# Performance work log

Hardware: AMD Instinct MI355X
Metric: run time of the kernel (lower is better)

The kernel has to match this reference:

```python
import jax, jax.numpy as jnp
import numpy as np

B, T, C, H = 2, 2048, 1024, 16
D = C // H  # head dim = 64


def setup_inputs() -> dict:
    key = jax.random.key(0)
    ks = jax.random.split(key, 9)
    s = 1.0 / np.sqrt(C)
    x = jax.random.normal(ks[0], (B, T, C), dtype=jnp.float32)
    # causal lower-triangular mask, broadcast over heads: [B, 1, T, T]
    attn_mask = jnp.broadcast_to(jnp.tril(jnp.ones((T, T), dtype=jnp.int32)), (B, 1, T, T))
    Wq = jax.random.normal(ks[1], (C, C), dtype=jnp.float32) * s
    Wk = jax.random.normal(ks[2], (C, C), dtype=jnp.float32) * s
    Wv = jax.random.normal(ks[3], (C, C), dtype=jnp.float32) * s
    Wo = jax.random.normal(ks[4], (C, C), dtype=jnp.float32) * s
    bq = jax.random.normal(ks[5], (C,), dtype=jnp.float32) * s
    bk = jax.random.normal(ks[6], (C,), dtype=jnp.float32) * s
    bv = jax.random.normal(ks[7], (C,), dtype=jnp.float32) * s
    bo = jax.random.normal(ks[8], (C,), dtype=jnp.float32) * s
    return {"x": x, "attn_mask": attn_mask, "Wq": Wq, "bq": bq, "Wk": Wk, "bk": bk,
            "Wv": Wv, "bv": bv, "Wo": Wo, "bo": bo}


def reference(x, attn_mask, Wq, bq, Wk, bk, Wv, bv, Wo, bo):
    # Q/K/V projections: nn.Linear applies x @ W^T + b
    def split_heads(t):  # [B,T,C] -> [B,H,T,D]
        return t.reshape(B, T, H, D).transpose(0, 2, 1, 3)

    q = split_heads(x @ Wq.T + bq)
    k = split_heads(x @ Wk.T + bk)
    v = split_heads(x @ Wv.T + bv)

    scale = 1.0 / np.sqrt(D)
    att = jnp.einsum('bhqd,bhkd->bhqk', q, k) * scale  # [B,H,T,T]
    att = jnp.where(attn_mask[:, :, :T, :T] == 0, -jnp.inf, att)
    att = jax.nn.softmax(att, axis=-1)
    # dropout p=0.0 -> identity
    y = jnp.einsum('bhqk,bhkd->bhqd', att, v)  # [B,H,T,D]
    y = y.transpose(0, 2, 1, 3).reshape(B, T, C)
    return y @ Wo.T + bo
```

## Files before the change

### kernel.cpp

```cpp
#include <hip/hip_runtime.h>
#include <hip/hip_bf16.h>

#define B_ 2
#define T_ 2048
#define C_ 1024
#define H_ 16
#define D_ 64
#define BT_ (B_ * T_)
#define S3_ 3072

typedef __bf16 bf16x8 __attribute__((ext_vector_type(8)));
typedef short short8v __attribute__((ext_vector_type(8)));
typedef short s16x4 __attribute__((ext_vector_type(4)));
typedef float f32x4 __attribute__((ext_vector_type(4)));

__device__ inline bf16x8 ld_frag_bf(const short* p) {
    short8v s = *(const short8v*)p;
    return __builtin_bit_cast(bf16x8, s);
}
__device__ inline short f2bf(float f) {
    union { float f; unsigned u; } x;
    x.f = f;
    unsigned r = x.u + 0x7fff + ((x.u >> 16) & 1);
    return (short)(r >> 16);
}
__device__ inline void st_out(short* p, float v) { *p = f2bf(v); }
__device__ inline void st_out(float* p, float v) { *p = v; }

__device__ inline void async16(const void* g, void* l) {
    __builtin_amdgcn_global_load_lds(
        (const __attribute__((address_space(1))) unsigned*)g,
        (__attribute__((address_space(3))) unsigned*)l, 16, 0, 0);
}

__global__ __launch_bounds__(256) void conv_inputs(
    const float* __restrict__ x,
    const float* __restrict__ Wq, const float* __restrict__ Wk,
    const float* __restrict__ Wv, const float* __restrict__ Wo,
    short* __restrict__ xb, short* __restrict__ Wqkvb, short* __restrict__ Wob)
{
    size_t e = ((size_t)blockIdx.x * 256 + threadIdx.x) * 8;
    int r = (int)(e >> 20);
    size_t off = e & ((1u << 20) - 1);
    const float* src; short* dst;
    if (r < 4)      { src = x + e;  dst = xb + e; }
    else if (r < 7) { src = (r == 4 ? Wq : r == 5 ? Wk : Wv) + off;
                      dst = Wqkvb + ((size_t)(r - 4) << 20) + off; }
    else            { src = Wo + off; dst = Wob + off; }
    f32x4 a = *(const f32x4*)src;
    f32x4 b = *(const f32x4*)(src + 4);
    short8v s;
#pragma unroll
    for (int i = 0; i < 4; ++i) { s[i] = f2bf(a[i]); s[i + 4] = f2bf(b[i]); }
    *(short8v*)dst = s;
}

__global__ __launch_bounds__(256) void gemm_qkv(
    const short* __restrict__ A,
    const short* __restrict__ Wb,
    const float* __restrict__ b0, const float* __restrict__ b1,
    const float* __restrict__ b2,
    short* __restrict__ Out, short* __restrict__ VQ)
{
    constexpr int K = 1024;
    __shared__ __align__(16) short Bs[128 * 64];
    __shared__ __align__(16) short As[128 * 64];

    const int tid = threadIdx.x;
    const int w = tid >> 6, l = tid & 63;
    const int c = l & 15, qd = l >> 4;
    const int m0 = blockIdx.y * 128, n0 = blockIdx.x * 128;
    const int wm = w >> 1, wn = w & 1;
    const int srcC = (l & 7) ^ (l >> 3);

    f32x4 acc[4][4] = {};

    for (int k0 = 0; k0 < K; k0 += 64) {
#pragma unroll
        for (int p = 0; p < 4; ++p) {
            int row = (w * 4 + p) * 8 + (l >> 3);
            async16(Wb + (size_t)(n0 + row) * K + k0 + srcC * 8,
                    Bs + (w * 4 + p) * 512 + l * 8);
            async16(A + (size_t)(m0 + row) * K + k0 + srcC * 8,
                    As + (w * 4 + p) * 512 + l * 8);
        }
        __syncthreads();

#pragma unroll
        for (int h = 0; h < 2; ++h) {
            const int slot = ((h * 4 + qd) ^ (c & 7)) * 8;
            bf16x8 af[4], bfr[4];
#pragma unroll
            for (int i = 0; i < 4; ++i) {
                af[i]  = ld_frag_bf(As + (wm * 64 + i * 16 + c) * 64 + slot);
                bfr[i] = ld_frag_bf(Bs + (wn * 64 + i * 16 + c) * 64 + slot);
            }
#pragma unroll
            for (int i = 0; i < 4; ++i)
#pragma unroll
                for (int j = 0; j < 4; ++j)
                    acc[i][j] = __builtin_amdgcn_mfma_f32_16x16x32_bf16(af[i], bfr[j], acc[i][j], 0, 0, 0);
        }
        __syncthreads();
    }

    if (n0 >= 2048) {
        const int h  = (n0 - 2048 + wn * 64) >> 6;
        const int b  = m0 >> 11;
        const int kt = ((m0 & 2047) + wm * 64) >> 6;
        short* vt = VQ + (((size_t)(b * 16 + h) * 32 + kt) * 4096);
#pragma unroll
        for (int i = 0; i < 4; ++i)
#pragma unroll
            for (int j = 0; j < 4; ++j) {
                float bv = b2[n0 - 2048 + wn * 64 + j * 16 + c];
                s16x4 st;
#pragma unroll
                for (int r = 0; r < 4; ++r) st[r] = f2bf(acc[i][j][r] + bv);
                *(s16x4*)&vt[((i * 4 + j) * 64 + qd * 16 + c) * 4] = st;
            }
    } else {
        const float* bias = (n0 < 1024) ? b0 : b1;
#pragma unroll
        for (int i = 0; i < 4; ++i)
#pragma unroll
            for (int j = 0; j < 4; ++j) {
                int n = n0 + wn * 64 + j * 16 + c;
                float bv = bias[n & 1023];
#pragma unroll
                for (int r = 0; r < 4; ++r) {
                    int m = m0 + wm * 64 + i * 16 + qd * 4 + r;
                    Out[(size_t)m * S3_ + n] = f2bf(acc[i][j][r] + bv);
                }
            }
    }
}

template <typename OT>
__global__ __launch_bounds__(256) void gemm_n64(
    const short* __restrict__ A, int lda,
    const short* __restrict__ Wb, const float* __restrict__ bias,
    OT* __restrict__ Out, int ldo)
{
    constexpr int K = 1024;
    __shared__ __align__(16) short Bs[64 * 64];
    __shared__ __align__(16) short As[128 * 64];

    const int tid = threadIdx.x;
    const int w = tid >> 6, l = tid & 63;
    const int c = l & 15, qd = l >> 4;
    const int m0 = blockIdx.y * 128, n0 = blockIdx.x * 64;
    const int wm = w >> 1, wn = w & 1;
    const int srcC = (l & 7) ^ (l >> 3);

    f32x4 acc[4][2] = {};

    for (int k0 = 0; k0 < K; k0 += 64) {
#pragma unroll
        for (int p = 0; p < 2; ++p) {
            int row = (w * 2 + p) * 8 + (l >> 3);
            async16(Wb + (size_t)(n0 + row) * K + k0 + srcC * 8,
                    Bs + (w * 2 + p) * 512 + l * 8);
        }
#pragma unroll
        for (int p = 0; p < 4; ++p) {
            int row = (w * 4 + p) * 8 + (l >> 3);
            async16(A + (size_t)(m0 + row) * lda + k0 + srcC * 8,
                    As + (w * 4 + p) * 512 + l * 8);
        }
        __syncthreads();

#pragma unroll
        for (int h = 0; h < 2; ++h) {
            const int slot = ((h * 4 + qd) ^ (c & 7)) * 8;
            bf16x8 af[4], bfr[2];
#pragma unroll
            for (int i = 0; i < 4; ++i)
                af[i] = ld_frag_bf(As + (wm * 64 + i * 16 + c) * 64 + slot);
#pragma unroll
            for (int j = 0; j < 2; ++j)
                bfr[j] = ld_frag_bf(Bs + (wn * 32 + j * 16 + c) * 64 + slot);
#pragma unroll
            for (int i = 0; i < 4; ++i)
#pragma unroll
                for (int j = 0; j < 2; ++j)
                    acc[i][j] = __builtin_amdgcn_mfma_f32_16x16x32_bf16(af[i], bfr[j], acc[i][j], 0, 0, 0);
        }
        __syncthreads();
    }

#pragma unroll
    for (int i = 0; i < 4; ++i)
#pragma unroll
        for (int j = 0; j < 2; ++j) {
            int n = n0 + wn * 32 + j * 16 + c;
            float bv = bias[n];
#pragma unroll
            for (int r = 0; r < 4; ++r) {
                int m = m0 + wm * 64 + i * 16 + qd * 4 + r;
                st_out(Out + (size_t)m * ldo + n, acc[i][j][r] + bv);
            }
        }
}

__global__ __launch_bounds__(256) void attn_flash7(
    short* __restrict__ QKV, const short* __restrict__ VQ)
{
    __shared__ __align__(16) short Ksm[2][4096];
    __shared__ __align__(16) short Vsm[2][4096];

    const int tid = threadIdx.x;
    const int w = tid >> 6, l = tid & 63;
    const int c = l & 15, qd = l >> 4;
    const int id = blockIdx.x;
    const int bh = (id & 7) * 4 + ((id >> 3) & 3);
    const int qt = 31 - (id >> 5);
    const int b = bh >> 4, h = bh & 15;
    const int sw = c & 7;

    short* Qbase = QKV + (size_t)b * T_ * S3_ + h * 64;
    const short* Kbase = Qbase + 1024;
    const short* VTb = VQ + (size_t)bh * 32 * 4096;

    const int wq0 = qt * 64 + w * 16;

    bf16x8 aq0 = ld_frag_bf(Qbase + (size_t)(wq0 + c) * S3_ + qd * 8);
    bf16x8 aq1 = ld_frag_bf(Qbase + (size_t)(wq0 + c) * S3_ + 32 + qd * 8);

    f32x4 o[4] = {};
    float lsum = 0.f;

#pragma unroll
    for (int p = 0; p < 2; ++p) {
        int row = p * 32 + w * 8 + (l >> 3);
        int srcC = (l & 7) ^ (row & 7);
        async16(Kbase + (size_t)row * S3_ + srcC * 8,
                &Ksm[0][row * 64 + (l & 7) * 8]);
        async16(VTb + p * 2048 + w * 512 + l * 8,
                &Vsm[0][p * 2048 + w * 512 + l * 8]);
    }
    __syncthreads();

#pragma unroll 1
    for (int kt = 0; kt <= qt; ++kt) {
        const int cur = kt & 1;
        const int k0 = kt * 64;

        if (kt < qt) {
            const short* vtile = VTb + (size_t)(kt + 1) * 4096;
#pragma unroll
            for (int p = 0; p < 2; ++p) {
                int row = p * 32 + w * 8 + (l >> 3);
                int srcC = (l & 7) ^ (row & 7);
                async16(Kbase + (size_t)(k0 + 64 + row) * S3_ + srcC * 8,
                        &Ksm[1 - cur][row * 64 + (l & 7) * 8]);
                async16(vtile + p * 2048 + w * 512 + l * 8,
                        &Vsm[1 - cur][p * 2048 + w * 512 + l * 8]);
            }
        }

        f32x4 st[4];
#pragma unroll
        for (int j = 0; j < 4; ++j) {
            st[j] = (f32x4){0.f, 0.f, 0.f, 0.f};
            const short* kr = &Ksm[cur][(j * 16 + c) * 64];
            bf16x8 kb0 = ld_frag_bf(kr + (qd ^ sw) * 8);
            bf16x8 kb1 = ld_frag_bf(kr + ((qd ^ 4) ^ sw) * 8);
            st[j] = __builtin_amdgcn_mfma_f32_16x16x32_bf16(kb0, aq0, st[j], 0, 0, 0);
            st[j] = __builtin_amdgcn_mfma_f32_16x16x32_bf16(kb1, aq1, st[j], 0, 0, 0);
        }

        s16x4 pb[4];
        if (kt < qt) {
#pragma unroll
            for (int j = 0; j < 4; ++j)
#pragma unroll
                for (int r = 0; r < 4; ++r) {
                    float p = __expf(fmaf(st[j][r], 0.125f, -8.0f));
                    lsum += p;
                    pb[j][r] = f2bf(p);
                }
        } else {
            const int qloc = w * 16 + c;
#pragma unroll
            for (int j = 0; j < 4; ++j)
#pragma unroll
                for (int r = 0; r < 4; ++r) {
                    float p = __expf(fmaf(st[j][r], 0.125f, -8.0f));
                    if (j * 16 + qd * 4 + r > qloc) p = 0.f;
                    lsum += p;
                    pb[j][r] = f2bf(p);
                }
        }

#pragma unroll
        for (int j = 0; j < 4; ++j)
#pragma unroll
            for (int i = 0; i < 4; ++i) {
                s16x4 vf = *(const s16x4*)&Vsm[cur][((j * 4 + i) * 64 + qd * 16 + c) * 4];
                o[i] = __builtin_amdgcn_mfma_f32_16x16x16bf16_1k(vf, pb[j], o[i], 0, 0, 0);
            }
        __syncthreads();
    }

    float lt = lsum;
    lt += __shfl_xor(lt, 16);
    lt += __shfl_xor(lt, 32);
    float inv = 1.0f / lt;

#pragma unroll
    for (int i = 0; i < 4; ++i) {
        s16x4 yb;
#pragma unroll
        for (int r = 0; r < 4; ++r) yb[r] = f2bf(o[i][r] * inv);
        *(s16x4*)&Qbase[(size_t)(wq0 + c) * S3_ + i * 16 + qd * 4] = yb;
    }
}

extern "C" void kernel_launch(void* const* d_in, const int* in_sizes, int n_in,
                              void* d_out, int out_size, void* d_ws, size_t ws_size,
                              hipStream_t stream)
{
    const float* x  = (const float*)d_in[0];
    const float* Wq = (const float*)d_in[2];
    const float* bq = (const float*)d_in[3];
    const float* Wk = (const float*)d_in[4];
    const float* bk = (const float*)d_in[5];
    const float* Wv = (const float*)d_in[6];
    const float* bv = (const float*)d_in[7];
    const float* Wo = (const float*)d_in[8];
    const float* bo = (const float*)d_in[9];
    float* out = (float*)d_out;

    short* QKVs  = (short*)d_ws;
    short* Wqkvb = QKVs + (size_t)BT_ * S3_;
    short* Wob   = Wqkvb + (size_t)S3_ * C_;
    short* xb    = (short*)d_out;
    short* VQ    = (short*)d_out + (size_t)4 * 1024 * 1024;

    conv_inputs<<<4096, 256, 0, stream>>>(x, Wq, Wk, Wv, Wo, xb, Wqkvb, Wob);
    gemm_qkv<<<dim3(S3_ / 128, BT_ / 128), 256, 0, stream>>>(
        xb, Wqkvb, bq, bk, bv, QKVs, VQ);
    attn_flash7<<<1024, 256, 0, stream>>>(QKVs, VQ);
    gemm_n64<float><<<dim3(C_ / 64, BT_ / 128), 256, 0, stream>>>(
        QKVs, S3_, Wob, bo, out, C_);
}
```

Before: 205.6 us.

## Double-buffer shared memory tiles in QKV and output projection GEMMs

Both GEMM kernels now keep two LDS buffers per operand and issue async loads for the next K-tile before running MFMAs on the current one. This is meant to overlap global-to-LDS transfers with matrix math instead of stalling at a barrier on every K step. The cost is double the shared memory per block, which can lower occupancy. Correctness depends on the async-copy completion semantics lining up with the barriers.

Result: slower. 219.5 us (+6.7%).

```diff
diff --git a/kernel.cpp b/kernel.cpp
--- a/kernel.cpp
+++ b/kernel.cpp
@@ -63,8 +63,8 @@
     short* __restrict__ Out, short* __restrict__ VQ)
 {
     constexpr int K = 1024;
-    __shared__ __align__(16) short Bs[128 * 64];
-    __shared__ __align__(16) short As[128 * 64];
+    __shared__ __align__(16) short Bs[2][128 * 64];
+    __shared__ __align__(16) short As[2][128 * 64];
 
     const int tid = threadIdx.x;
     const int w = tid >> 6, l = tid & 63;
@@ -75,25 +75,25 @@
 
     f32x4 acc[4][4] = {};
 
-    for (int k0 = 0; k0 < K; k0 += 64) {
+    auto stage = [&](short* Asb, short* Bsb, int k0) {
 #pragma unroll
         for (int p = 0; p < 4; ++p) {
             int row = (w * 4 + p) * 8 + (l >> 3);
             async16(Wb + (size_t)(n0 + row) * K + k0 + srcC * 8,
-                    Bs + (w * 4 + p) * 512 + l * 8);
+                    Bsb + (w * 4 + p) * 512 + l * 8);
             async16(A + (size_t)(m0 + row) * K + k0 + srcC * 8,
-                    As + (w * 4 + p) * 512 + l * 8);
-        }
-        __syncthreads();
-
+                    Asb + (w * 4 + p) * 512 + l * 8);
+        }
+    };
+    auto compute = [&](const short* Asb, const short* Bsb) {
 #pragma unroll
         for (int h = 0; h < 2; ++h) {
             const int slot = ((h * 4 + qd) ^ (c & 7)) * 8;
             bf16x8 af[4], bfr[4];
 #pragma unroll
             for (int i = 0; i < 4; ++i) {
-                af[i]  = ld_frag_bf(As + (wm * 64 + i * 16 + c) * 64 + slot);
-                bfr[i] = ld_frag_bf(Bs + (wn * 64 + i * 16 + c) * 64 + slot);
+                af[i]  = ld_frag_bf(Asb + (wm * 64 + i * 16 + c) * 64 + slot);
+                bfr[i] = ld_frag_bf(Bsb + (wn * 64 + i * 16 + c) * 64 + slot);
             }
 #pragma unroll
             for (int i = 0; i < 4; ++i)
@@ -101,6 +101,19 @@
                 for (int j = 0; j < 4; ++j)
                     acc[i][j] = __builtin_amdgcn_mfma_f32_16x16x32_bf16(af[i], bfr[j], acc[i][j], 0, 0, 0);
         }
+    };
+
+    stage(As[0], Bs[0], 0);
+    __syncthreads();
+
+#pragma unroll 1
+    for (int k0 = 0; k0 < K; k0 += 128) {
+        stage(As[1], Bs[1], k0 + 64);
+        compute(As[0], Bs[0]);
+        __syncthreads();
+        if (k0 + 128 < K)
+            stage(As[0], Bs[0], k0 + 128);
+        compute(As[1], Bs[1]);
         __syncthreads();
     }
 
@@ -143,8 +156,8 @@
     OT* __restrict__ Out, int ldo)
 {
     constexpr int K = 1024;
-    __shared__ __align__(16) short Bs[64 * 64];
-    __shared__ __align__(16) short As[128 * 64];
+    __shared__ __align__(16) short Bs[2][64 * 64];
+    __shared__ __align__(16) short As[2][128 * 64];
 
     const int tid = threadIdx.x;
     const int w = tid >> 6, l = tid & 63;
@@ -155,37 +168,50 @@
 
     f32x4 acc[4][2] = {};
 
-    for (int k0 = 0; k0 < K; k0 += 64) {
+    auto stage = [&](short* Asb, short* Bsb, int k0) {
 #pragma unroll
         for (int p = 0; p < 2; ++p) {
             int row = (w * 2 + p) * 8 + (l >> 3);
             async16(Wb + (size_t)(n0 + row) * K + k0 + srcC * 8,
-                    Bs + (w * 2 + p) * 512 + l * 8);
+                    Bsb + (w * 2 + p) * 512 + l * 8);
         }
 #pragma unroll
         for (int p = 0; p < 4; ++p) {
             int row = (w * 4 + p) * 8 + (l >> 3);
             async16(A + (size_t)(m0 + row) * lda + k0 + srcC * 8,
-                    As + (w * 4 + p) * 512 + l * 8);
-        }
-        __syncthreads();
-
+                    Asb + (w * 4 + p) * 512 + l * 8);
+        }
+    };
+    auto compute = [&](const short* Asb, const short* Bsb) {
 #pragma unroll
         for (int h = 0; h < 2; ++h) {
             const int slot = ((h * 4 + qd) ^ (c & 7)) * 8;
             bf16x8 af[4], bfr[2];
 #pragma unroll
             for (int i = 0; i < 4; ++i)
-                af[i] = ld_frag_bf(As + (wm * 64 + i * 16 + c) * 64 + slot);
+                af[i] = ld_frag_bf(Asb + (wm * 64 + i * 16 + c) * 64 + slot);
 #pragma unroll
             for (int j = 0; j < 2; ++j)
-                bfr[j] = ld_frag_bf(Bs + (wn * 32 + j * 16 + c) * 64 + slot);
+                bfr[j] = ld_frag_bf(Bsb + (wn * 32 + j * 16 + c) * 64 + slot);
 #pragma unroll
             for (int i = 0; i < 4; ++i)
 #pragma unroll
                 for (int j = 0; j < 2; ++j)
                     acc[i][j] = __builtin_amdgcn_mfma_f32_16x16x32_bf16(af[i], bfr[j], acc[i][j], 0, 0, 0);
         }
+    };
+
+    stage(As[0], Bs[0], 0);
+    __syncthreads();
+
+#pragma unroll 1
+    for (int k0 = 0; k0 < K; k0 += 128) {
+        stage(As[1], Bs[1], k0 + 64);
+        compute(As[0], Bs[0]);
+        __syncthreads();
+        if (k0 + 128 < K)
+            stage(As[0], Bs[0], k0 + 128);
+        compute(As[1], Bs[1]);
         __syncthreads();
     }
 
```

## Double-buffer QKV GEMM shared tiles with half-K stages to overlap loads

Applied to the files above, without the earlier changes.

Splits the 64-wide K tile of the QKV projection GEMM into two 32-wide shared-memory buffers and stages the next half-tile asynchronously while MFMAs run on the current one. It also changes the LDS layout and swizzle to suit the 32-column tiles. The goal is to hide global-to-LDS load latency behind compute instead of stalling at a barrier every iteration. The cost is an extra barrier per 64-K step and a more intricate swizzle that must stay bank-conflict free.

After: 210.9 us. 2.6% more time.

```diff
diff --git a/kernel.cpp b/kernel.cpp
--- a/kernel.cpp
+++ b/kernel.cpp
@@ -63,44 +63,60 @@
     short* __restrict__ Out, short* __restrict__ VQ)
 {
     constexpr int K = 1024;
-    __shared__ __align__(16) short Bs[128 * 64];
-    __shared__ __align__(16) short As[128 * 64];
+    __shared__ __align__(16) short Bs[2][128 * 32];
+    __shared__ __align__(16) short As[2][128 * 32];
 
     const int tid = threadIdx.x;
     const int w = tid >> 6, l = tid & 63;
     const int c = l & 15, qd = l >> 4;
     const int m0 = blockIdx.y * 128, n0 = blockIdx.x * 128;
     const int wm = w >> 1, wn = w & 1;
-    const int srcC = (l & 7) ^ (l >> 3);
+
+    const int u    = (l & 7) ^ (l >> 3);
+    const int sb   = (u >> 2) & 1;
+    const int sch8 = (u & 3) * 8;
+    const int srow = (l >> 3) * 2 + sb;
+
+    const int pslot   = (((c & 1) << 2) + qd) ^ (c >> 1);
+    const int colbase = (c >> 1) * 64 + pslot * 8;
 
     f32x4 acc[4][4] = {};
 
+    auto stage = [&](int buf, int k0) {
+#pragma unroll
+        for (int k = 0; k < 2; ++k) {
+            int row = (w * 2 + k) * 16 + srow;
+            async16(Wb + (size_t)(n0 + row) * K + k0 + sch8,
+                    &Bs[buf][(w * 2 + k) * 512 + l * 8]);
+            async16(A + (size_t)(m0 + row) * K + k0 + sch8,
+                    &As[buf][(w * 2 + k) * 512 + l * 8]);
+        }
+    };
+    auto compute = [&](int buf) {
+        bf16x8 af[4], bfr[4];
+#pragma unroll
+        for (int i = 0; i < 4; ++i) {
+            af[i]  = ld_frag_bf(&As[buf][wm * 2048 + i * 512 + colbase]);
+            bfr[i] = ld_frag_bf(&Bs[buf][wn * 2048 + i * 512 + colbase]);
+        }
+#pragma unroll
+        for (int i = 0; i < 4; ++i)
+#pragma unroll
+            for (int j = 0; j < 4; ++j)
+                acc[i][j] = __builtin_amdgcn_mfma_f32_16x16x32_bf16(af[i], bfr[j], acc[i][j], 0, 0, 0);
+    };
+
+    stage(0, 0);
+    __syncthreads();
+
+#pragma unroll 1
     for (int k0 = 0; k0 < K; k0 += 64) {
-#pragma unroll
-        for (int p = 0; p < 4; ++p) {
-            int row = (w * 4 + p) * 8 + (l >> 3);
-            async16(Wb + (size_t)(n0 + row) * K + k0 + srcC * 8,
-                    Bs + (w * 4 + p) * 512 + l * 8);
-            async16(A + (size_t)(m0 + row) * K + k0 + srcC * 8,
-                    As + (w * 4 + p) * 512 + l * 8);
-        }
-        __syncthreads();
-
-#pragma unroll
-        for (int h = 0; h < 2; ++h) {
-            const int slot = ((h * 4 + qd) ^ (c & 7)) * 8;
-            bf16x8 af[4], bfr[4];
-#pragma unroll
-            for (int i = 0; i < 4; ++i) {
-                af[i]  = ld_frag_bf(As + (wm * 64 + i * 16 + c) * 64 + slot);
-                bfr[i] = ld_frag_bf(Bs + (wn * 64 + i * 16 + c) * 64 + slot);
-            }
-#pragma unroll
-            for (int i = 0; i < 4; ++i)
-#pragma unroll
-                for (int j = 0; j < 4; ++j)
-                    acc[i][j] = __builtin_amdgcn_mfma_f32_16x16x32_bf16(af[i], bfr[j], acc[i][j], 0, 0, 0);
-        }
+        stage(1, k0 + 32);
+        compute(0);
+        __syncthreads();
+        if (k0 + 64 < K)
+            stage(0, k0 + 64);
+        compute(1);
         __syncthreads();
     }
 
```
